# Performance work log

Measured on AMD Instinct MI355X. Metric: run time of the kernel, lower is better.

The kernel has to match this reference:

```python
import jax, jax.numpy as jnp
import numpy as np

GROUPS = 16
EPS = 1e-5


def _gn_sigmoid_branch(y, w1, b1, gamma, beta):
    # y: [b, c, L] -> Conv1d 1x1 -> GroupNorm(16) -> sigmoid
    z = jnp.einsum('bcl,dc->bdl', y, w1) + b1[None, :, None]
    b, c, L = z.shape
    zg = z.reshape(b, GROUPS, c // GROUPS, L)
    mu = zg.mean(axis=(2, 3), keepdims=True)
    var = zg.var(axis=(2, 3), keepdims=True)
    zn = ((zg - mu) * jax.lax.rsqrt(var + EPS)).reshape(b, c, L)
    return jax.nn.sigmoid(zn * gamma[None, :, None] + beta[None, :, None])


def setup_inputs() -> dict:
    key = jax.random.key(0)
    ks = jax.random.split(key, 4)
    b, c, h, w = 8, 256, 64, 64
    x = jax.random.normal(ks[0], (b, c, h, w), dtype=jnp.float32)
    w_qkv = jax.random.normal(ks[1], (3 * c, c), dtype=jnp.float32) * (c ** -0.5)
    w1 = jax.random.normal(ks[2], (c, c), dtype=jnp.float32) * (c ** -0.5)
    b1 = jax.random.normal(ks[3], (c,), dtype=jnp.float32) * 0.02
    gn_gamma = jnp.ones((c,), dtype=jnp.float32)
    gn_beta = jnp.zeros((c,), dtype=jnp.float32)
    return {"x": x, "w_qkv": w_qkv, "w1": w1, "b1": b1,
            "gn_gamma": gn_gamma, "gn_beta": gn_beta}


def reference(x, w_qkv, w1, b1, gn_gamma, gn_beta):
    b, c, h, w = x.shape
    scale = c ** (-0.5)
    # ELA gating branch (conv1x1/GN/sigmoid shared between h- and w-pooled paths)
    x_h = _gn_sigmoid_branch(x.mean(axis=3), w1, b1, gn_gamma, gn_beta)  # [b,c,h]
    x_w = _gn_sigmoid_branch(x.mean(axis=2), w1, b1, gn_gamma, gn_beta)  # [b,c,w]
    ela_out = x * x_h[:, :, :, None] * x_w[:, :, None, :]
    # full spatial self-attention
    qkv = jnp.einsum('bchw,dc->bdhw', x, w_qkv).reshape(b, 3 * c, h * w)
    q, k, v = qkv[:, :c], qkv[:, c:2 * c], qkv[:, 2 * c:]  # each [b,c,hw]
    attn = jax.nn.softmax(jnp.einsum('bcn,bcm->bnm', q, k) * scale, axis=-1)
    softmax_out = jnp.einsum('bnm,bcm->bcn', attn, v).reshape(b, c, h, w)
    return ela_out + softmax_out
```

## Files before the change

kernel.cpp:

```cpp
#include <hip/hip_runtime.h>

typedef __bf16 bf16;
typedef float f32x4 __attribute__((ext_vector_type(4)));
typedef float f32x2 __attribute__((ext_vector_type(2)));
typedef __bf16 bf16x8 __attribute__((ext_vector_type(8)));
typedef __bf16 bf16x4 __attribute__((ext_vector_type(4)));

#define NB 8
#define NC 256
#define NL 64
#define NN 4096

__device__ __forceinline__ void gl_lds16(const bf16* g, bf16* l) {
    __builtin_amdgcn_global_load_lds(
        (const __attribute__((address_space(1))) unsigned int*)g,
        (__attribute__((address_space(3))) unsigned int*)l, 16, 0, 0);
}

__device__ __forceinline__ float fexp2(float x) {
#if __has_builtin(__builtin_amdgcn_exp2f)
    return __builtin_amdgcn_exp2f(x);
#else
    return exp2f(x);
#endif
}

#define QSCALE (0.0625f * 1.44269504f)

__global__ void cast_w_kernel(const float* __restrict__ w, bf16* __restrict__ wb) {
    int i = (blockIdx.x * 256 + threadIdx.x) * 4;
    f32x4 v = *(const f32x4*)(w + i);
    bf16x4 o;
    o[0] = (bf16)v[0]; o[1] = (bf16)v[1]; o[2] = (bf16)v[2]; o[3] = (bf16)v[3];
    *(bf16x4*)(wb + i) = o;
}

__global__ void transpose_kernel(const float* __restrict__ x, bf16* __restrict__ xT) {
    __shared__ __align__(16) bf16 ls[256 * 68];
    int n0 = blockIdx.x * 64;
    int b = blockIdx.y;
    const float* xp = x + (size_t)b * NC * NN + n0;
    int t = threadIdx.x;
    #pragma unroll
    for (int i = 0; i < 16; ++i) {
        int chunk = t + i * 256;
        int c = chunk >> 4, k4 = (chunk & 15) * 4;
        f32x4 v = *(const f32x4*)(xp + (size_t)c * NN + k4);
        bf16x4 o;
        o[0] = (bf16)v[0]; o[1] = (bf16)v[1]; o[2] = (bf16)v[2]; o[3] = (bf16)v[3];
        *(bf16x4*)&ls[c * 68 + k4] = o;
    }
    __syncthreads();
    bf16* xo = xT + ((size_t)b * NN + n0) * NC;
    #pragma unroll
    for (int i = 0; i < 8; ++i) {
        int chunk = t + i * 256;
        int n = chunk >> 5, c0 = (chunk & 31) * 8;
        bf16x8 o;
        #pragma unroll
        for (int j = 0; j < 8; ++j) o[j] = ls[(c0 + j) * 68 + n];
        *(bf16x8*)(xo + (size_t)n * NC + c0) = o;
    }
}

__global__ __launch_bounds__(256) void meansT_kernel(const bf16* __restrict__ xT,
                                                     float* __restrict__ xh,
                                                     float* __restrict__ xw) {
    __shared__ float red[8][256];
    int b = blockIdx.y;
    int m = blockIdx.x;
    int hmode = (m < 64);
    int fix = hmode ? m : m - 64;
    int t = threadIdx.x;
    int c8 = (t & 31) * 8, g = t >> 5;
    float acc[8] = {0.f, 0.f, 0.f, 0.f, 0.f, 0.f, 0.f, 0.f};
    #pragma unroll
    for (int pass = 0; pass < 8; ++pass) {
        int r = g + pass * 8;
        int n = hmode ? fix * 64 + r : r * 64 + fix;
        bf16x8 v = *(const bf16x8*)(xT + ((size_t)b * NN + n) * NC + c8);
        #pragma unroll
        for (int j = 0; j < 8; ++j) acc[j] += (float)v[j];
    }
    #pragma unroll
    for (int j = 0; j < 8; ++j) red[g][c8 + j] = acc[j];
    __syncthreads();
    float s = red[0][t] + red[1][t] + red[2][t] + red[3][t]
            + red[4][t] + red[5][t] + red[6][t] + red[7][t];
    float* dst = hmode ? xh : xw;
    dst[((size_t)b * NC + t) * NL + fix] = s * (1.f / 64.f);
}

__global__ void branch_kernel(const float* __restrict__ xh_m, const float* __restrict__ xw_m,
                              const float* __restrict__ w1, const float* __restrict__ b1,
                              const float* __restrict__ gamma, const float* __restrict__ beta,
                              float* __restrict__ x_h, float* __restrict__ x_w) {
    __shared__ float ys[NC * NL];
    int id = blockIdx.x;
    int g = id & 15, br = (id >> 4) & 1, b = id >> 5;
    const float* y = (br ? xw_m : xh_m) + (size_t)b * NC * NL;
    float* outp = (br ? x_w : x_h) + (size_t)b * NC * NL;
    int t = threadIdx.x;
    #pragma unroll
    for (int i = 0; i < 16; ++i) {
        int idx = (t + i * 256) * 4;
        *(f32x4*)&ys[idx] = *(const f32x4*)&y[idx];
    }
    __syncthreads();
    int l = t & 63;
    int dq = __builtin_amdgcn_readfirstlane(t >> 6);
    float z[4];
    #pragma unroll
    for (int k = 0; k < 4; ++k) z[k] = b1[g * 16 + dq + 4 * k];
    for (int c = 0; c < 256; ++c) {
        float yv = ys[c * 64 + l];
        #pragma unroll
        for (int k = 0; k < 4; ++k) z[k] += w1[(g * 16 + dq + 4 * k) * 256 + c] * yv;
    }
    float s1 = z[0] + z[1] + z[2] + z[3];
    float s2 = z[0] * z[0] + z[1] * z[1] + z[2] * z[2] + z[3] * z[3];
    #pragma unroll
    for (int off = 1; off < 64; off <<= 1) {
        s1 += __shfl_xor(s1, off);
        s2 += __shfl_xor(s2, off);
    }
    __syncthreads();
    if (l == 0) { ys[dq * 2] = s1; ys[dq * 2 + 1] = s2; }
    __syncthreads();
    s1 = ys[0] + ys[2] + ys[4] + ys[6];
    s2 = ys[1] + ys[3] + ys[5] + ys[7];
    float mean = s1 * (1.f / 1024.f);
    float var = s2 * (1.f / 1024.f) - mean * mean;
    float rs = rsqrtf(var + 1e-5f);
    #pragma unroll
    for (int k = 0; k < 4; ++k) {
        int d = g * 16 + dq + 4 * k;
        float zn = (z[k] - mean) * rs;
        float tt = zn * gamma[d] + beta[d];
        outp[(size_t)d * NL + l] = 1.f / (1.f + __expf(-tt));
    }
}

__global__ __launch_bounds__(256) void qkv_kernel(
        const bf16* __restrict__ xT, const bf16* __restrict__ wb,
        bf16* __restrict__ Q, bf16* __restrict__ K, bf16* __restrict__ V) {
    int b = blockIdx.x & 7;
    int n0 = (blockIdx.x >> 3) * 64;
    int d0 = blockIdx.y * 64;
    int t = threadIdx.x;
    int wave = t >> 6, lane = t & 63, l15 = lane & 15, quad = lane >> 4;
    const bf16* ap = xT + ((size_t)b * NN + n0 + wave * 16 + l15) * NC + quad * 8;
    const bf16* bp = wb + (size_t)(d0 + l15) * NC + quad * 8;
    f32x4 acc[4];
    #pragma unroll
    for (int dt = 0; dt < 4; ++dt) acc[dt] = f32x4{0.f, 0.f, 0.f, 0.f};
    #pragma unroll
    for (int kc = 0; kc < 8; ++kc) {
        bf16x8 a = *(const bf16x8*)(ap + kc * 32);
        #pragma unroll
        for (int dt = 0; dt < 4; ++dt) {
            bf16x8 bb = *(const bf16x8*)(bp + (size_t)dt * 16 * NC + kc * 32);
            acc[dt] = __builtin_amdgcn_mfma_f32_16x16x32_bf16(a, bb, acc[dt], 0, 0, 0);
        }
    }
    int nbase = n0 + wave * 16 + quad * 4;
    #pragma unroll
    for (int dt = 0; dt < 4; ++dt) {
        int d = d0 + dt * 16 + l15;
        if (d < 256) {
            #pragma unroll
            for (int r = 0; r < 4; ++r)
                Q[((size_t)b * NN + nbase + r) * NC + d] = (bf16)(acc[dt][r] * QSCALE);
        } else if (d < 512) {
            #pragma unroll
            for (int r = 0; r < 4; ++r)
                K[((size_t)b * NN + nbase + r) * NC + (d - 256)] = (bf16)acc[dt][r];
        } else {
            bf16x4 pv;
            #pragma unroll
            for (int r = 0; r < 4; ++r) pv[r] = (bf16)acc[dt][r];
            *(bf16x4*)(V + ((size_t)b * NC + (d - 512)) * NN + nbase) = pv;
        }
    }
}

__global__ __launch_bounds__(256, 2) void flash_kernel(
        const bf16* __restrict__ Q, const bf16* __restrict__ Kg, const bf16* __restrict__ V,
        bf16* __restrict__ Opart, float* __restrict__ lsum) {
    __shared__ __align__(16) bf16 Ks[2][32 * 256];
    __shared__ __align__(16) bf16 Vs[2][256 * 32];
    __shared__ __align__(16) bf16 Ps[4][32 * 40];
    int id = blockIdx.x;
    int b = id & 7, split = (id >> 3) & 1, qt = id >> 4;
    int n0 = qt * 128;
    int t = threadIdx.x;
    int wave = t >> 6, lane = t & 63, l15 = lane & 15, quad = lane >> 4;

    const bf16* kbase = Kg + (size_t)b * NN * NC;
    const bf16* vbase = V + (size_t)b * NC * NN;

    int krow_l = (wave << 3) + (lane >> 5);
    int kgp = lane & 31;
    int vd_l = (wave << 6) + (lane >> 2);
    int vkp = lane & 3;

    bf16x8 qf[2][8];
    #pragma unroll
    for (int mt = 0; mt < 2; ++mt) {
        const bf16* qp = Q + ((size_t)b * NN + n0 + wave * 32 + mt * 16 + l15) * NC + quad * 8;
        #pragma unroll
        for (int kc = 0; kc < 8; ++kc) qf[mt][kc] = *(const bf16x8*)(qp + kc * 32);
    }

    f32x4 oacc[2][16];
    #pragma unroll
    for (int mt = 0; mt < 2; ++mt)
        #pragma unroll
        for (int dt = 0; dt < 16; ++dt) oacc[mt][dt] = f32x4{0.f, 0.f, 0.f, 0.f};
    float li[2] = {0.f, 0.f};

    auto issue = [&](int kt, int buf) {
        int key0 = (split * 64 + kt) * 32;
        bf16* kdst = &Ks[buf][wave * 2048];
        bf16* vdst = &Vs[buf][wave * 2048];
        #pragma unroll
        for (int i = 0; i < 4; ++i) {
            int krow = krow_l + i * 2;
            gl_lds16(kbase + (size_t)(key0 + krow) * NC + ((kgp ^ (krow & 7)) << 3),
                     kdst + i * 512);
            int vd = vd_l + i * 16;
            gl_lds16(vbase + (size_t)vd * NN + key0 + (((vkp - (vd >> 1)) & 3) << 3),
                     vdst + i * 512);
        }
    };

    issue(0, 0);
    for (int kt = 0; kt < 64; ++kt) {
        int cur = kt & 1;
        __syncthreads();
        if (kt < 63) issue(kt + 1, cur ^ 1);
        const bf16* ks = Ks[cur];
        const bf16* vs = Vs[cur];

        f32x4 s[2][2];
        s[0][0] = f32x4{0.f,0.f,0.f,0.f}; s[0][1] = f32x4{0.f,0.f,0.f,0.f};
        s[1][0] = f32x4{0.f,0.f,0.f,0.f}; s[1][1] = f32x4{0.f,0.f,0.f,0.f};
        #pragma unroll
        for (int kc = 0; kc < 8; ++kc) {
            #pragma unroll
            for (int nt = 0; nt < 2; ++nt) {
                int r = nt * 16 + l15;
                bf16x8 kf = *(const bf16x8*)&ks[r * NC + (((kc * 4 + quad) ^ (r & 7)) << 3)];
                s[0][nt] = __builtin_amdgcn_mfma_f32_16x16x32_bf16(kf, qf[0][kc], s[0][nt], 0, 0, 0);
                s[1][nt] = __builtin_amdgcn_mfma_f32_16x16x32_bf16(kf, qf[1][kc], s[1][nt], 0, 0, 0);
            }
        }

        #pragma unroll
        for (int mt = 0; mt < 2; ++mt) {
            float p0[4], p1[4];
            #pragma unroll
            for (int r = 0; r < 4; ++r) {
                p0[r] = fexp2(s[mt][0][r]);
                p1[r] = fexp2(s[mt][1][r]);
            }
            li[mt] += (p0[0] + p0[1]) + (p0[2] + p0[3])
                    + (p1[0] + p1[1]) + (p1[2] + p1[3]);
            bf16x4 w0, w1;
            #pragma unroll
            for (int r = 0; r < 4; ++r) { w0[r] = (bf16)p0[r]; w1[r] = (bf16)p1[r]; }
            *(bf16x4*)&Ps[wave][(mt * 16 + l15) * 40 + quad * 4] = w0;
            *(bf16x4*)&Ps[wave][(mt * 16 + l15) * 40 + 16 + quad * 4] = w1;
        }
        bf16x8 pf0 = *(const bf16x8*)&Ps[wave][l15 * 40 + quad * 8];
        bf16x8 pf1 = *(const bf16x8*)&Ps[wave][(16 + l15) * 40 + quad * 8];
        #pragma unroll
        for (int dt = 0; dt < 16; ++dt) {
            int d = dt * 16 + l15;
            bf16x8 vf = *(const bf16x8*)&vs[(d << 5) + (((quad + (d >> 1)) & 3) << 3)];
            oacc[0][dt] = __builtin_amdgcn_mfma_f32_16x16x32_bf16(pf0, vf, oacc[0][dt], 0, 0, 0);
            oacc[1][dt] = __builtin_amdgcn_mfma_f32_16x16x32_bf16(pf1, vf, oacc[1][dt], 0, 0, 0);
        }
    }

    bf16* op = Opart + (size_t)(split * NB + b) * NN * NC;
    #pragma unroll
    for (int mt = 0; mt < 2; ++mt) {
        float v = li[mt];
        v += __shfl_xor(v, 16);
        v += __shfl_xor(v, 32);
        if (quad == 0)
            lsum[(size_t)(split * NB + b) * NN + n0 + wave * 32 + mt * 16 + l15] = v;
        int nrow = n0 + wave * 32 + mt * 16 + quad * 4;
        #pragma unroll
        for (int dt = 0; dt < 16; ++dt) {
            #pragma unroll
            for (int r = 0; r < 4; ++r)
                op[(size_t)(nrow + r) * NC + dt * 16 + l15] = (bf16)oacc[mt][dt][r];
        }
    }
}

__global__ __launch_bounds__(256) void combine_kernel(
        const bf16* __restrict__ Opart, const float* __restrict__ lsum,
        const float* __restrict__ x, const float* __restrict__ x_h,
        const float* __restrict__ x_w, float* __restrict__ out) {
    __shared__ float ts[64 * 65];
    int h = blockIdx.x, b = blockIdx.y;
    int n0 = h * 64;
    int t = threadIdx.x;
    const size_t oso = (size_t)NB * NN * NC;
    const size_t lso = (size_t)NB * NN;
    for (int c = 0; c < 4; ++c) {
        int d0 = c * 64;
        if (c) __syncthreads();
        #pragma unroll
        for (int i = 0; i < 4; ++i) {
            int n = i * 16 + (t >> 4);
            int dq = (t & 15) * 4;
            size_t obase = ((size_t)b * NN + n0 + n) * NC + d0 + dq;
            bf16x4 o1 = *(const bf16x4*)(Opart + obase);
            bf16x4 o2 = *(const bf16x4*)(Opart + oso + obase);
            size_t lb = (size_t)b * NN + n0 + n;
            float inv = 1.f / (lsum[lb] + lsum[lso + lb]);
            #pragma unroll
            for (int j = 0; j < 4; ++j)
                ts[(dq + j) * 65 + n] = ((float)o1[j] + (float)o2[j]) * inv;
        }
        __syncthreads();
        #pragma unroll
        for (int i = 0; i < 4; ++i) {
            int dd = i * 16 + (t >> 4);
            int nq = (t & 15) * 4;
            int d = d0 + dd;
            size_t cb = (size_t)b * NC + d;
            f32x4 xv = *(const f32x4*)(x + cb * NN + n0 + nq);
            float xhv = x_h[cb * NL + h];
            f32x4 xwv = *(const f32x4*)(x_w + cb * NL + nq);
            f32x4 o;
            #pragma unroll
            for (int j = 0; j < 4; ++j)
                o[j] = ts[dd * 65 + nq + j] + xv[j] * xhv * xwv[j];
            *(f32x4*)(out + cb * NN + n0 + nq) = o;
        }
    }
}

extern "C" void kernel_launch(void* const* d_in, const int* in_sizes, int n_in,
                              void* d_out, int out_size, void* d_ws, size_t ws_size,
                              hipStream_t stream) {
    const float* x      = (const float*)d_in[0];
    const float* w_qkv  = (const float*)d_in[1];
    const float* w1     = (const float*)d_in[2];
    const float* b1     = (const float*)d_in[3];
    const float* gamma  = (const float*)d_in[4];
    const float* beta   = (const float*)d_in[5];
    float* out = (float*)d_out;

    char* ws = (char*)d_ws;
    bf16*  xT    = (bf16*)(ws);
    bf16*  Qw    = (bf16*)(ws + 16777216);
    bf16*  Kw    = (bf16*)(ws + 33554432);
    bf16*  Vw    = (bf16*)(ws + 50331648);
    bf16*  wb    = (bf16*)(ws + 67108864);
    float* xh_m  = (float*)(ws + 67502080);
    float* xw_m  = (float*)(ws + 68026368);
    float* x_h   = (float*)(ws + 68550656);
    float* x_w   = (float*)(ws + 69074944);
    bf16*  Opart = (bf16*)(ws + 69599232);
    float* lsb   = (float*)(ws + 103153664);

    hipLaunchKernelGGL(cast_w_kernel, dim3(192), dim3(256), 0, stream, w_qkv, wb);
    hipLaunchKernelGGL(transpose_kernel, dim3(64, 8), dim3(256), 0, stream, x, xT);
    hipLaunchKernelGGL(meansT_kernel, dim3(128, 8), dim3(256), 0, stream, xT, xh_m, xw_m);
    hipLaunchKernelGGL(branch_kernel, dim3(256), dim3(256), 0, stream,
                       xh_m, xw_m, w1, b1, gamma, beta, x_h, x_w);
    hipLaunchKernelGGL(qkv_kernel, dim3(512, 12), dim3(256), 0, stream, xT, wb, Qw, Kw, Vw);
    hipLaunchKernelGGL(flash_kernel, dim3(512), dim3(256), 0, stream,
                       Qw, Kw, Vw, Opart, lsb);
    hipLaunchKernelGGL(combine_kernel, dim3(64, 8), dim3(256), 0, stream,
                       Opart, lsb, x, x_h, x_w, out);
}
```

Baseline: 377.0 us.

## Fuse h-means into transpose, merge weight cast with w-means, stage QKV weights in LDS

The h-direction pooling is computed inside the transpose kernel from the tile already held in shared memory, which removes a separate pass over xT. The weight cast to bf16 is folded into the w-means kernel as extra blocks, cutting one kernel launch. The QKV projection now stages its 64-row weight tile in LDS and preloads the A fragments into registers, instead of reading weights from global memory for every MFMA. This costs more shared memory and registers, and adds a block-wide sync in the QKV kernel.

After: 312.6 us. 17.1% less time.

```diff
diff --git a/kernel.cpp b/kernel.cpp
--- a/kernel.cpp
+++ b/kernel.cpp
@@ -27,17 +27,11 @@
 
 #define QSCALE (0.0625f * 1.44269504f)
 
-__global__ void cast_w_kernel(const float* __restrict__ w, bf16* __restrict__ wb) {
-    int i = (blockIdx.x * 256 + threadIdx.x) * 4;
-    f32x4 v = *(const f32x4*)(w + i);
-    bf16x4 o;
-    o[0] = (bf16)v[0]; o[1] = (bf16)v[1]; o[2] = (bf16)v[2]; o[3] = (bf16)v[3];
-    *(bf16x4*)(wb + i) = o;
-}
-
-__global__ void transpose_kernel(const float* __restrict__ x, bf16* __restrict__ xT) {
+__global__ void transpose_kernel(const float* __restrict__ x, bf16* __restrict__ xT,
+                                 float* __restrict__ xh) {
     __shared__ __align__(16) bf16 ls[256 * 68];
-    int n0 = blockIdx.x * 64;
+    int h = blockIdx.x;
+    int n0 = h * 64;
     int b = blockIdx.y;
     const float* xp = x + (size_t)b * NC * NN + n0;
     int t = threadIdx.x;
@@ -61,23 +55,39 @@
         for (int j = 0; j < 8; ++j) o[j] = ls[(c0 + j) * 68 + n];
         *(bf16x8*)(xo + (size_t)n * NC + c0) = o;
     }
-}
-
-__global__ __launch_bounds__(256) void meansT_kernel(const bf16* __restrict__ xT,
-                                                     float* __restrict__ xh,
-                                                     float* __restrict__ xw) {
-    __shared__ float red[8][256];
+    float s = 0.f;
+    #pragma unroll 8
+    for (int j = 0; j < 64; ++j) s += (float)ls[t * 68 + j];
+    xh[((size_t)b * NC + t) * NL + h] = s * (1.f / 64.f);
+}
+
+__global__ __launch_bounds__(256) void meansw_cast_kernel(
+        const bf16* __restrict__ xT, float* __restrict__ xw,
+        const float* __restrict__ w, bf16* __restrict__ wb) {
     int b = blockIdx.y;
     int m = blockIdx.x;
-    int hmode = (m < 64);
-    int fix = hmode ? m : m - 64;
-    int t = threadIdx.x;
+    int t = threadIdx.x;
+    if (m >= 64) {
+        if (b != 0) return;
+        int blk = m - 64;
+        #pragma unroll
+        for (int jj = 0; jj < 8; ++jj) {
+            int i = blk * 8192 + jj * 1024 + t * 4;
+            f32x4 v = *(const f32x4*)(w + i);
+            bf16x4 o;
+            o[0] = (bf16)v[0]; o[1] = (bf16)v[1]; o[2] = (bf16)v[2]; o[3] = (bf16)v[3];
+            *(bf16x4*)(wb + i) = o;
+        }
+        return;
+    }
+    __shared__ float red[8][256];
+    int fix = m;
     int c8 = (t & 31) * 8, g = t >> 5;
     float acc[8] = {0.f, 0.f, 0.f, 0.f, 0.f, 0.f, 0.f, 0.f};
     #pragma unroll
     for (int pass = 0; pass < 8; ++pass) {
         int r = g + pass * 8;
-        int n = hmode ? fix * 64 + r : r * 64 + fix;
+        int n = r * 64 + fix;
         bf16x8 v = *(const bf16x8*)(xT + ((size_t)b * NN + n) * NC + c8);
         #pragma unroll
         for (int j = 0; j < 8; ++j) acc[j] += (float)v[j];
@@ -87,8 +97,7 @@
     __syncthreads();
     float s = red[0][t] + red[1][t] + red[2][t] + red[3][t]
             + red[4][t] + red[5][t] + red[6][t] + red[7][t];
-    float* dst = hmode ? xh : xw;
-    dst[((size_t)b * NC + t) * NL + fix] = s * (1.f / 64.f);
+    xw[((size_t)b * NC + t) * NL + fix] = s * (1.f / 64.f);
 }
 
 __global__ void branch_kernel(const float* __restrict__ xh_m, const float* __restrict__ xw_m,
@@ -144,23 +153,37 @@
 __global__ __launch_bounds__(256) void qkv_kernel(
         const bf16* __restrict__ xT, const bf16* __restrict__ wb,
         bf16* __restrict__ Q, bf16* __restrict__ K, bf16* __restrict__ V) {
+    __shared__ __align__(16) bf16 wbs[64 * 264];
     int b = blockIdx.x & 7;
     int n0 = (blockIdx.x >> 3) * 64;
     int d0 = blockIdx.y * 64;
     int t = threadIdx.x;
     int wave = t >> 6, lane = t & 63, l15 = lane & 15, quad = lane >> 4;
+
     const bf16* ap = xT + ((size_t)b * NN + n0 + wave * 16 + l15) * NC + quad * 8;
-    const bf16* bp = wb + (size_t)(d0 + l15) * NC + quad * 8;
+    bf16x8 a[8];
+    #pragma unroll
+    for (int kc = 0; kc < 8; ++kc) a[kc] = *(const bf16x8*)(ap + kc * 32);
+
+    {
+        int row = t & 63, chunk = t >> 6;
+        const bf16* gp = wb + (size_t)(d0 + row) * NC + chunk * 64;
+        bf16* lp = &wbs[row * 264 + chunk * 64];
+        #pragma unroll
+        for (int j = 0; j < 8; ++j)
+            *(bf16x8*)(lp + j * 8) = *(const bf16x8*)(gp + j * 8);
+    }
+    __syncthreads();
+
     f32x4 acc[4];
     #pragma unroll
     for (int dt = 0; dt < 4; ++dt) acc[dt] = f32x4{0.f, 0.f, 0.f, 0.f};
     #pragma unroll
     for (int kc = 0; kc < 8; ++kc) {
-        bf16x8 a = *(const bf16x8*)(ap + kc * 32);
         #pragma unroll
         for (int dt = 0; dt < 4; ++dt) {
-            bf16x8 bb = *(const bf16x8*)(bp + (size_t)dt * 16 * NC + kc * 32);
-            acc[dt] = __builtin_amdgcn_mfma_f32_16x16x32_bf16(a, bb, acc[dt], 0, 0, 0);
+            bf16x8 bb = *(const bf16x8*)&wbs[(dt * 16 + l15) * 264 + kc * 32 + quad * 8];
+            acc[dt] = __builtin_amdgcn_mfma_f32_16x16x32_bf16(a[kc], bb, acc[dt], 0, 0, 0);
         }
     }
     int nbase = n0 + wave * 16 + quad * 4;
@@ -370,9 +393,9 @@
     bf16*  Opart = (bf16*)(ws + 69599232);
     float* lsb   = (float*)(ws + 103153664);
 
-    hipLaunchKernelGGL(cast_w_kernel, dim3(192), dim3(256), 0, stream, w_qkv, wb);
-    hipLaunchKernelGGL(transpose_kernel, dim3(64, 8), dim3(256), 0, stream, x, xT);
-    hipLaunchKernelGGL(meansT_kernel, dim3(128, 8), dim3(256), 0, stream, xT, xh_m, xw_m);
+    hipLaunchKernelGGL(transpose_kernel, dim3(64, 8), dim3(256), 0, stream, x, xT, xh_m);
+    hipLaunchKernelGGL(meansw_cast_kernel, dim3(88, 8), dim3(256), 0, stream,
+                       xT, xw_m, w_qkv, wb);
     hipLaunchKernelGGL(branch_kernel, dim3(256), dim3(256), 0, stream,
                        xh_m, xw_m, w1, b1, gamma, beta, x_h, x_w);
     hipLaunchKernelGGL(qkv_kernel, dim3(512, 12), dim3(256), 0, stream, xT, wb, Qw, Kw, Vw);
```
